# Optimization experiments

Measured on AMD Instinct MI355X. Metric: run time of the kernel, lower is better.

## Reference

```python
import jax, jax.numpy as jnp
import numpy as np

N = 100000  # nodes
E = 500000  # directed edges (before self-loops)

def _glorot(key, fi, fo):
    s = np.sqrt(6.0 / (fi + fo)).astype(np.float32)
    return jax.random.uniform(key, (fi, fo), jnp.float32, -s, s)

def setup_inputs() -> dict:
    key = jax.random.key(0)
    ks = jax.random.split(key, 6)
    x = jax.random.normal(ks[0], (N, 128), jnp.float32)
    edge_index = jax.random.randint(ks[1], (2, E), 0, N, dtype=jnp.int64)
    return {
        "x": x,
        "edge_index": edge_index,
        "W1": _glorot(ks[2], 128, 512), "b1": jnp.zeros((512,), jnp.float32),
        "W2": _glorot(ks[3], 512, 768), "b2": jnp.zeros((768,), jnp.float32),
        "W3": _glorot(ks[4], 768, 512), "b3": jnp.zeros((512,), jnp.float32),
        "W4": _glorot(ks[5], 512, 128), "b4": jnp.zeros((128,), jnp.float32),
    }

def reference(x, edge_index, W1, b1, W2, b2, W3, b3, W4, b4):
    # PyG GCNConv: add self-loops, deg from dst index, sym-normalized scatter-add.
    loops = jnp.arange(N, dtype=edge_index.dtype)
    src = jnp.concatenate([edge_index[0], loops])  # [E+N]
    dst = jnp.concatenate([edge_index[1], loops])  # [E+N]
    deg = jax.ops.segment_sum(jnp.ones_like(dst, jnp.float32), dst, num_segments=N)
    dinv = jax.lax.rsqrt(deg)  # deg >= 1 thanks to self-loops
    norm = (dinv[src] * dinv[dst])[:, None]  # [E+N, 1]

    def gcn_conv(h, W, b):
        hw = h @ W                                  # [N, Fout] dense linear
        msg = norm * hw[src]                        # [E+N, Fout] gather + scale
        return jax.ops.segment_sum(msg, dst, num_segments=N) + b

    h = jax.nn.gelu(gcn_conv(x, W1, b1), approximate=False)
    h = jax.nn.gelu(gcn_conv(h, W2, b2), approximate=False)
    h = jax.nn.gelu(gcn_conv(h, W3, b3), approximate=False)
    return gcn_conv(h, W4, b4)
```

## Files before the change

### kernel.cpp

```cpp
#include <hip/hip_runtime.h>

typedef short bf16x8 __attribute__((ext_vector_type(8)));
typedef float f32x4 __attribute__((ext_vector_type(4)));

__device__ __forceinline__ float b2f(unsigned short u) {
  union { unsigned int i; float f; } x; x.i = ((unsigned int)u) << 16; return x.f;
}
__device__ __forceinline__ unsigned short f2b(float f) {
  union { float f; unsigned int u; } x; x.f = f;
  unsigned int r = (x.u + 0x7FFFu + ((x.u >> 16) & 1u)) >> 16;
  return (unsigned short)r;
}
__device__ __forceinline__ float gelu_f(float v) {
  return 0.5f * v * (1.0f + erff(v * 0.70710678118654752440f));
}


__global__ void count_kernel(const int* __restrict__ ei, int E, int* __restrict__ cnt) {
  int e = blockIdx.x * 256 + threadIdx.x;
  if (e < E) atomicAdd(&cnt[ei[E + e]], 1);
}

__global__ void dinv_kernel(const int* __restrict__ cnt, float* __restrict__ dinv, int Nn) {
  int n = blockIdx.x * 256 + threadIdx.x;
  if (n < Nn) dinv[n] = rsqrtf((float)cnt[n] + 1.0f);
}


__global__ __launch_bounds__(256) void scanA_kernel(const int* __restrict__ cnt,
                                                    int* __restrict__ bsum, int Nn) {
  __shared__ int red[256];
  const int t = threadIdx.x;
  const int base = blockIdx.x * 512 + t * 2;
  int a = (base < Nn) ? cnt[base] : 0;
  int b = (base + 1 < Nn) ? cnt[base + 1] : 0;
  red[t] = a + b;
  __syncthreads();
  for (int d = 128; d > 0; d >>= 1) {
    if (t < d) red[t] += red[t + d];
    __syncthreads();
  }
  if (t == 0) bsum[blockIdx.x] = red[0];
}

__global__ __launch_bounds__(256) void scanB_kernel(const int* __restrict__ bsum,
                                                    int* __restrict__ boff,
                                                    int* __restrict__ rowstart,
                                                    int NBLK, int Nn) {
  __shared__ int sh[256];
  const int t = threadIdx.x;
  sh[t] = (t < NBLK) ? bsum[t] : 0;
  __syncthreads();
  for (int d = 1; d < 256; d <<= 1) {
    int x = sh[t];
    int add = (t >= d) ? sh[t - d] : 0;
    __syncthreads();
    sh[t] = x + add;
    __syncthreads();
  }
  if (t < NBLK) boff[t] = (t == 0) ? 0 : sh[t - 1];
  if (t == NBLK - 1) rowstart[Nn] = sh[t];
}

__global__ __launch_bounds__(256) void scanC_kernel(const int* __restrict__ cnt,
                                                    const int* __restrict__ boff,
                                                    int* __restrict__ rowstart,
                                                    int* __restrict__ cursor, int Nn) {
  __shared__ int sh[256];
  const int t = threadIdx.x;
  const int base = blockIdx.x * 512 + t * 2;
  int a = (base < Nn) ? cnt[base] : 0;
  int b = (base + 1 < Nn) ? cnt[base + 1] : 0;
  sh[t] = a + b;
  __syncthreads();
  for (int d = 1; d < 256; d <<= 1) {
    int x = sh[t];
    int add = (t >= d) ? sh[t - d] : 0;
    __syncthreads();
    sh[t] = x + add;
    __syncthreads();
  }
  const int off = boff[blockIdx.x] + ((t == 0) ? 0 : sh[t - 1]);
  if (base < Nn) { rowstart[base] = off; cursor[base] = off; }
  if (base + 1 < Nn) { rowstart[base + 1] = off + a; cursor[base + 1] = off + a; }
}

__global__ void fill_kernel(const int* __restrict__ ei, int E, const float* __restrict__ dinv,
                            int* __restrict__ cursor, int* __restrict__ ssrc,
                            float* __restrict__ snorm) {
  int e = blockIdx.x * 256 + threadIdx.x;
  if (e < E) {
    int s = ei[e], d = ei[E + e];
    int pos = atomicAdd(&cursor[d], 1);
    ssrc[pos] = s;
    snorm[pos] = dinv[s] * dinv[d];
  }
}

__global__ void wtrans_kernel(const float* __restrict__ W, unsigned short* __restrict__ WT,
                              int K, int N) {
  int i = blockIdx.x * 256 + threadIdx.x;
  if (i < K * N) {
    int n = i / K, k = i - n * K;
    WT[i] = f2b(W[k * N + n]);
  }
}


template <int F, bool INF32, bool OUTF32, bool HASBIAS, bool DOGELU>
__global__ __launch_bounds__(256) void agg_kernel(
    const int* __restrict__ rowstart, const int* __restrict__ ssrc,
    const float* __restrict__ snorm, const float* __restrict__ dinv,
    const void* __restrict__ inv, const float* __restrict__ bias,
    void* __restrict__ outv, int Nn) {
  constexpr int V = F / 64;
  const int lane = threadIdx.x & 63;
  const int node = blockIdx.x * 4 + (threadIdx.x >> 6);
  if (node >= Nn) return;
  const int base = lane * V;
  float acc[V];
  {
    float w = dinv[node]; w = w * w;
    if constexpr (INF32) {
      const float* in = (const float*)inv + (size_t)node * F + base;
      if constexpr (V == 2) {
        float2 v = *(const float2*)in; acc[0] = w * v.x; acc[1] = w * v.y;
      } else {
        float4 v0 = *(const float4*)in; float4 v1 = *(const float4*)(in + 4);
        acc[0] = w * v0.x; acc[1] = w * v0.y; acc[2] = w * v0.z; acc[3] = w * v0.w;
        acc[4] = w * v1.x; acc[5] = w * v1.y; acc[6] = w * v1.z; acc[7] = w * v1.w;
      }
    } else {
      const unsigned short* in = (const unsigned short*)inv + (size_t)node * F + base;
      if constexpr (V == 2) {
        unsigned int v = *(const unsigned int*)in;
        acc[0] = w * b2f(v & 0xffffu); acc[1] = w * b2f(v >> 16);
      } else {
        bf16x8 v = *(const bf16x8*)in;
#pragma unroll
        for (int i = 0; i < 8; ++i) acc[i] = w * b2f((unsigned short)v[i]);
      }
    }
  }
  const int e0 = rowstart[node], e1 = rowstart[node + 1];
  for (int e = e0; e < e1; ++e) {
    const int s = ssrc[e];
    const float w = snorm[e];
    if constexpr (INF32) {
      const float* in = (const float*)inv + (size_t)s * F + base;
      if constexpr (V == 2) {
        float2 v = *(const float2*)in; acc[0] += w * v.x; acc[1] += w * v.y;
      } else {
        float4 v0 = *(const float4*)in; float4 v1 = *(const float4*)(in + 4);
        acc[0] += w * v0.x; acc[1] += w * v0.y; acc[2] += w * v0.z; acc[3] += w * v0.w;
        acc[4] += w * v1.x; acc[5] += w * v1.y; acc[6] += w * v1.z; acc[7] += w * v1.w;
      }
    } else {
      const unsigned short* in = (const unsigned short*)inv + (size_t)s * F + base;
      if constexpr (V == 2) {
        unsigned int v = *(const unsigned int*)in;
        acc[0] += w * b2f(v & 0xffffu); acc[1] += w * b2f(v >> 16);
      } else {
        bf16x8 v = *(const bf16x8*)in;
#pragma unroll
        for (int i = 0; i < 8; ++i) acc[i] += w * b2f((unsigned short)v[i]);
      }
    }
  }
  if constexpr (HASBIAS) {
#pragma unroll
    for (int i = 0; i < V; ++i) acc[i] += bias[base + i];
  }
  if constexpr (DOGELU) {
#pragma unroll
    for (int i = 0; i < V; ++i) acc[i] = gelu_f(acc[i]);
  }
  if constexpr (OUTF32) {
    float* out = (float*)outv + (size_t)node * F + base;
#pragma unroll
    for (int i = 0; i < V; ++i) out[i] = acc[i];
  } else {
    unsigned short* out = (unsigned short*)outv + (size_t)node * F + base;
    if constexpr (V == 2) {
      unsigned int pack = (unsigned int)f2b(acc[0]) | ((unsigned int)f2b(acc[1]) << 16);
      *(unsigned int*)out = pack;
    } else {
      bf16x8 o;
#pragma unroll
      for (int i = 0; i < 8; ++i) o[i] = (short)f2b(acc[i]);
      *(bf16x8*)out = o;
    }
  }
}


template <bool HASBIAS, bool DOGELU>
__global__ __launch_bounds__(512, 2) void gemm256(
    const unsigned short* __restrict__ A, const unsigned short* __restrict__ BT,
    const float* __restrict__ bias, unsigned short* __restrict__ C,
    int N, int K, int NT) {
  __shared__ alignas(16) unsigned short smem[65536];
  unsigned short* As = smem;
  unsigned short* Bs = smem + 32768;
  const int tid = threadIdx.x;
  const int lane = tid & 63;
  const int wid = tid >> 6;
  const int wr = wid >> 2;
  const int wc = wid & 3;
  const int rr = lane & 15, rg = lane >> 4;

  const int G = gridDim.x;
  const int q = G >> 3, r = G & 7;
  const int xcd = blockIdx.x & 7, ii = blockIdx.x >> 3;
  const int w = (xcd < r ? xcd * (q + 1) : r * (q + 1) + (xcd - r) * q) + ii;
  const int bx = w / NT;
  const int by = w - bx * NT;
  const size_t brow = (size_t)bx * 256;
  const size_t bcol = (size_t)by * 256;

  const int nt = K >> 6;

  auto stage = [&](int t) {
    const int kb = t << 6;
    const int buf = t & 1;
#pragma unroll
    for (int j = 0; j < 4; ++j) {
      const int s = tid + 512 * j;
      const int row = s >> 3;
      const int lslot = (s & 7) ^ (row & 7);
      const unsigned short* gA = A + (brow + row) * K + kb + lslot * 8;
      __builtin_amdgcn_global_load_lds((const __attribute__((address_space(1))) void*)gA,
          (__attribute__((address_space(3))) void*)(&As[buf * 16384 + s * 8]), 16, 0, 0);
      const unsigned short* gB = BT + (bcol + row) * K + kb + lslot * 8;
      __builtin_amdgcn_global_load_lds((const __attribute__((address_space(1))) void*)gB,
          (__attribute__((address_space(3))) void*)(&Bs[buf * 16384 + s * 8]), 16, 0, 0);
    }
  };

  f32x4 acc[8][4] = {};
  stage(0);
  __syncthreads();
  for (int t = 0; t < nt; ++t) {
    if (t + 1 < nt) stage(t + 1);
    const int buf = t & 1;
    bf16x8 bq[2][4];
#pragma unroll
    for (int kk = 0; kk < 2; ++kk)
#pragma unroll
      for (int nb = 0; nb < 4; ++nb) {
        const int R = wc * 64 + nb * 16 + rr;
        const int ps = (kk * 4 + rg) ^ (R & 7);
        bq[kk][nb] = *(const bf16x8*)(&Bs[buf * 16384 + R * 64 + ps * 8]);
      }
#pragma unroll
    for (int mb = 0; mb < 8; ++mb) {
      const int R = wr * 128 + mb * 16 + rr;
      const int ps0 = rg ^ (R & 7);
      const int ps1 = (4 + rg) ^ (R & 7);
      bf16x8 a0 = *(const bf16x8*)(&As[buf * 16384 + R * 64 + ps0 * 8]);
      bf16x8 a1 = *(const bf16x8*)(&As[buf * 16384 + R * 64 + ps1 * 8]);
#pragma unroll
      for (int nb = 0; nb < 4; ++nb)
        acc[mb][nb] = __builtin_amdgcn_mfma_f32_16x16x32_bf16(a0, bq[0][nb], acc[mb][nb], 0, 0, 0);
#pragma unroll
      for (int nb = 0; nb < 4; ++nb)
        acc[mb][nb] = __builtin_amdgcn_mfma_f32_16x16x32_bf16(a1, bq[1][nb], acc[mb][nb], 0, 0, 0);
    }
    __syncthreads();
  }

  char* Cl = (char*)smem;
#pragma unroll
  for (int mb = 0; mb < 8; ++mb) {
    const int rowl0 = wr * 128 + mb * 16 + rg * 4;
#pragma unroll
    for (int nb = 0; nb < 4; ++nb) {
      const int coll = wc * 64 + nb * 16 + rr;
      float bv = 0.0f;
      if constexpr (HASBIAS) bv = bias[bcol + coll];
#pragma unroll
      for (int r2 = 0; r2 < 4; ++r2) {
        float v = acc[mb][nb][r2] + bv;
        if constexpr (DOGELU) v = gelu_f(v);
        const int rowl = rowl0 + r2;
        *(unsigned short*)(Cl + rowl * 512 + ((coll * 2) ^ ((rowl & 7) << 4))) = f2b(v);
      }
    }
  }
  __syncthreads();
#pragma unroll
  for (int pass = 0; pass < 2; ++pass) {
    const int rowl = pass * 128 + (tid >> 2);
    const int u = tid & 3;
    const size_t gbase = (brow + rowl) * (size_t)N + bcol;
#pragma unroll
    for (int c = 0; c < 8; ++c) {
      uint4 v = *(const uint4*)(Cl + rowl * 512 + ((c * 64 + u * 16) ^ ((rowl & 7) << 4)));
      *(uint4*)(&C[gbase + c * 32 + u * 8]) = v;
    }
  }
}


template <bool HASBIAS, bool DOGELU>
__global__ __launch_bounds__(256) void gemm_bt(
    const unsigned short* __restrict__ A, const unsigned short* __restrict__ BT,
    const float* __restrict__ bias, unsigned short* __restrict__ C,
    int N, int K, int NT) {
  __shared__ alignas(16) unsigned short Asl[128 * 32];
  __shared__ alignas(16) unsigned short Bsl[128 * 32];
  const int tid = threadIdx.x;
  const int lane = tid & 63;
  const int wid = tid >> 6;

  const int G = gridDim.x;
  const int q = G >> 3, r = G & 7;
  const int xcd = blockIdx.x & 7, ii = blockIdx.x >> 3;
  const int w = (xcd < r ? xcd * (q + 1) : r * (q + 1) + (xcd - r) * q) + ii;
  const int bx = w / NT;
  const int by = w - bx * NT;

  const size_t brow = (size_t)bx * 128;
  const size_t bcol = (size_t)by * 128;
  const int wr = (wid >> 1) * 64;
  const int wc = (wid & 1) * 64;
  const int rr = lane & 15, rg = lane >> 4;
  f32x4 acc[4][4] = {};
  const int KT = K >> 5;
  for (int kt = 0; kt < KT; ++kt) {
    const int kb = kt << 5;
#pragma unroll
    for (int rsub = 0; rsub < 2; ++rsub) {
      const int c = tid + rsub * 256;
      const int arow = c >> 2;
      const int jlog = (c & 3) ^ ((arow >> 1) & 3);
      const unsigned short* gA = A + (brow + arow) * K + kb + jlog * 8;
      __builtin_amdgcn_global_load_lds((const __attribute__((address_space(1))) void*)gA,
                                       (__attribute__((address_space(3))) void*)(&Asl[c * 8]),
                                       16, 0, 0);
      const unsigned short* gB = BT + (bcol + arow) * K + kb + jlog * 8;
      __builtin_amdgcn_global_load_lds((const __attribute__((address_space(1))) void*)gB,
                                       (__attribute__((address_space(3))) void*)(&Bsl[c * 8]),
                                       16, 0, 0);
    }
    __syncthreads();
    bf16x8 af[4], bfr[4];
#pragma unroll
    for (int m = 0; m < 4; ++m) {
      const int R = wr + m * 16 + rr;
      af[m] = *(const bf16x8*)(&Asl[R * 32 + ((rg ^ ((R >> 1) & 3)) * 8)]);
    }
#pragma unroll
    for (int n = 0; n < 4; ++n) {
      const int R = wc + n * 16 + rr;
      bfr[n] = *(const bf16x8*)(&Bsl[R * 32 + ((rg ^ ((R >> 1) & 3)) * 8)]);
    }
#pragma unroll
    for (int m = 0; m < 4; ++m)
#pragma unroll
      for (int n = 0; n < 4; ++n)
        acc[m][n] = __builtin_amdgcn_mfma_f32_16x16x32_bf16(af[m], bfr[n], acc[m][n], 0, 0, 0);
    __syncthreads();
  }
#pragma unroll
  for (int m = 0; m < 4; ++m) {
    size_t row0 = brow + wr + m * 16 + rg * 4;
#pragma unroll
    for (int n = 0; n < 4; ++n) {
      size_t col = bcol + wc + n * 16 + rr;
      float bv = 0.0f;
      if constexpr (HASBIAS) bv = bias[col];
#pragma unroll
      for (int r2 = 0; r2 < 4; ++r2) {
        float v = acc[m][n][r2] + bv;
        if constexpr (DOGELU) v = gelu_f(v);
        C[(row0 + r2) * N + col] = f2b(v);
      }
    }
  }
}


extern "C" void kernel_launch(void* const* d_in, const int* in_sizes, int n_in,
                              void* d_out, int out_size, void* d_ws, size_t ws_size,
                              hipStream_t stream) {
  const float* x = (const float*)d_in[0];
  const int* ei = (const int*)d_in[1];
  const float* W1 = (const float*)d_in[2]; const float* b1 = (const float*)d_in[3];
  const float* W2 = (const float*)d_in[4]; const float* b2 = (const float*)d_in[5];
  const float* W3 = (const float*)d_in[6]; const float* b3 = (const float*)d_in[7];
  const float* W4 = (const float*)d_in[8]; const float* b4 = (const float*)d_in[9];

  const int Nn = in_sizes[0] / 128;
  const int E = in_sizes[1] / 2;
  const int Mpad = (Nn + 255) & ~255;

  char* p = (char*)d_ws;
  auto alloc = [&](size_t bytes) {
    char* r = p;
    p += (bytes + 255) & ~(size_t)255;
    return r;
  };
  float* dinv = (float*)alloc((size_t)Nn * 4);
  int* cnt = (int*)alloc((size_t)Nn * 4);
  int* rowstart = (int*)alloc((size_t)(Nn + 1) * 4);
  int* cursor = (int*)alloc((size_t)Nn * 4);
  int* ssrc = (int*)alloc((size_t)E * 4);
  float* snorm = (float*)alloc((size_t)E * 4);
  int* bsum = (int*)alloc((size_t)256 * 4);
  int* boff = (int*)alloc((size_t)256 * 4);
  unsigned short* WT1 = (unsigned short*)alloc((size_t)512 * 128 * 2);
  unsigned short* WT2 = (unsigned short*)alloc((size_t)768 * 512 * 2);
  unsigned short* WT3 = (unsigned short*)alloc((size_t)512 * 768 * 2);
  unsigned short* WT4 = (unsigned short*)alloc((size_t)128 * 512 * 2);
  unsigned short* bufA = (unsigned short*)alloc((size_t)Mpad * 512 * 2);
  unsigned short* bufB = (unsigned short*)alloc((size_t)Mpad * 768 * 2);

  const int EB = (E + 255) / 256;
  const int NB = (Nn + 255) / 256;
  const int AGGB = (Nn + 3) / 4;
  const int MT128 = Mpad / 128;
  const int MT256 = Mpad / 256;
  const int NSCAN = (Nn + 511) / 512;

  hipMemsetAsync(cnt, 0, (size_t)Nn * 4, stream);
  count_kernel<<<EB, 256, 0, stream>>>(ei, E, cnt);
  dinv_kernel<<<NB, 256, 0, stream>>>(cnt, dinv, Nn);
  scanA_kernel<<<NSCAN, 256, 0, stream>>>(cnt, bsum, Nn);
  scanB_kernel<<<1, 256, 0, stream>>>(bsum, boff, rowstart, NSCAN, Nn);
  scanC_kernel<<<NSCAN, 256, 0, stream>>>(cnt, boff, rowstart, cursor, Nn);
  fill_kernel<<<EB, 256, 0, stream>>>(ei, E, dinv, cursor, ssrc, snorm);
  wtrans_kernel<<<(128 * 512 + 255) / 256, 256, 0, stream>>>(W1, WT1, 128, 512);
  wtrans_kernel<<<(512 * 768 + 255) / 256, 256, 0, stream>>>(W2, WT2, 512, 768);
  wtrans_kernel<<<(768 * 512 + 255) / 256, 256, 0, stream>>>(W3, WT3, 768, 512);
  wtrans_kernel<<<(512 * 128 + 255) / 256, 256, 0, stream>>>(W4, WT4, 512, 128);

  agg_kernel<128, true, false, false, false><<<AGGB, 256, 0, stream>>>(
      rowstart, ssrc, snorm, dinv, x, nullptr, bufA, Nn);
  gemm256<true, true><<<MT256 * 2, 512, 0, stream>>>(bufA, WT1, b1, bufB, 512, 128, 2);

  agg_kernel<512, false, false, false, false><<<AGGB, 256, 0, stream>>>(
      rowstart, ssrc, snorm, dinv, bufB, nullptr, bufA, Nn);
  gemm256<true, true><<<MT256 * 3, 512, 0, stream>>>(bufA, WT2, b2, bufB, 768, 512, 3);

  gemm256<false, false><<<MT256 * 2, 512, 0, stream>>>(bufB, WT3, nullptr, bufA, 512, 768, 2);
  agg_kernel<512, false, false, true, true><<<AGGB, 256, 0, stream>>>(
      rowstart, ssrc, snorm, dinv, bufA, b3, bufB, Nn);

  gemm_bt<false, false><<<MT128 * 1, 256, 0, stream>>>(bufB, WT4, nullptr, bufA, 128, 512, 1);
  agg_kernel<128, false, true, true, false><<<AGGB, 256, 0, stream>>>(
      rowstart, ssrc, snorm, dinv, bufA, b4, d_out, Nn);
}
```

Measured before the change: 781.9 us.

## Restructure gemm256 main loop into fine-grained phased pipeline with explicit waitcnts

The 256x256 GEMM main loop is rewritten as eight phases per 128-wide K step. Each phase loads a quarter-size A or B half-tile into LDS while the MFMAs for the previous sub-tile run, using explicit vmcnt waits, raw s_barrier and s_setprio instead of one full-tile prefetch followed by __syncthreads. The LDS layout changes to 32-wide K halves with a new XOR swizzle, and launch bounds drop to one block per CU to free registers. The goal is to hide global-to-LDS latency and barrier stalls behind MFMA work. The hand-counted waitcnt scheme assumes K is a multiple of 128 and the exact number of loads in flight, so it is fragile.

```diff
diff --git a/kernel.cpp b/kernel.cpp
--- a/kernel.cpp
+++ b/kernel.cpp
@@ -194,14 +194,16 @@
 }
 
 
+#define GLOAD16(gp, lp)                                                              \
+  __builtin_amdgcn_global_load_lds((const __attribute__((address_space(1))) void*)(gp), \
+                                   (__attribute__((address_space(3))) void*)(lp), 16, 0, 0)
+
 template <bool HASBIAS, bool DOGELU>
-__global__ __launch_bounds__(512, 2) void gemm256(
+__global__ __launch_bounds__(512, 1) void gemm256(
     const unsigned short* __restrict__ A, const unsigned short* __restrict__ BT,
     const float* __restrict__ bias, unsigned short* __restrict__ C,
     int N, int K, int NT) {
   __shared__ alignas(16) unsigned short smem[65536];
-  unsigned short* As = smem;
-  unsigned short* Bs = smem + 32768;
   const int tid = threadIdx.x;
   const int lane = tid & 63;
   const int wid = tid >> 6;
@@ -218,56 +220,94 @@
   const size_t brow = (size_t)bx * 256;
   const size_t bcol = (size_t)by * 256;
 
-  const int nt = K >> 6;
-
-  auto stage = [&](int t) {
-    const int kb = t << 6;
-    const int buf = t & 1;
-#pragma unroll
-    for (int j = 0; j < 4; ++j) {
+  const int ntiles = K >> 6;
+  const int NIT = K >> 7;
+
+  auto stageA = [&](int tl, int h) {
+    if (tl >= ntiles) return;
+    const int kb = (tl << 6) + (h << 5);
+    unsigned short* dst = smem + ((tl & 1) * 2 + h) * 8192;
+#pragma unroll
+    for (int j = 0; j < 2; ++j) {
       const int s = tid + 512 * j;
-      const int row = s >> 3;
-      const int lslot = (s & 7) ^ (row & 7);
-      const unsigned short* gA = A + (brow + row) * K + kb + lslot * 8;
-      __builtin_amdgcn_global_load_lds((const __attribute__((address_space(1))) void*)gA,
-          (__attribute__((address_space(3))) void*)(&As[buf * 16384 + s * 8]), 16, 0, 0);
-      const unsigned short* gB = BT + (bcol + row) * K + kb + lslot * 8;
-      __builtin_amdgcn_global_load_lds((const __attribute__((address_space(1))) void*)gB,
-          (__attribute__((address_space(3))) void*)(&Bs[buf * 16384 + s * 8]), 16, 0, 0);
+      const int row = s >> 2;
+      const int kof = (((s & 3) ^ ((row >> 1) & 3)) << 3);
+      GLOAD16(A + (brow + row) * K + kb + kof, dst + s * 8);
     }
   };
+  auto stageB = [&](int tl, int h) {
+    if (tl >= ntiles) return;
+    const int kb = (tl << 6) + (h << 5);
+    unsigned short* dst = smem + 32768 + ((tl & 1) * 2 + h) * 8192;
+#pragma unroll
+    for (int j = 0; j < 2; ++j) {
+      const int s = tid + 512 * j;
+      const int row = s >> 2;
+      const int kof = (((s & 3) ^ ((row >> 1) & 3)) << 3);
+      GLOAD16(BT + (bcol + row) * K + kb + kof, dst + s * 8);
+    }
+  };
 
   f32x4 acc[8][4] = {};
-  stage(0);
-  __syncthreads();
-  for (int t = 0; t < nt; ++t) {
-    if (t + 1 < nt) stage(t + 1);
-    const int buf = t & 1;
-    bf16x8 bq[2][4];
-#pragma unroll
-    for (int kk = 0; kk < 2; ++kk)
-#pragma unroll
-      for (int nb = 0; nb < 4; ++nb) {
-        const int R = wc * 64 + nb * 16 + rr;
-        const int ps = (kk * 4 + rg) ^ (R & 7);
-        bq[kk][nb] = *(const bf16x8*)(&Bs[buf * 16384 + R * 64 + ps * 8]);
-      }
-#pragma unroll
-    for (int mb = 0; mb < 8; ++mb) {
-      const int R = wr * 128 + mb * 16 + rr;
-      const int ps0 = rg ^ (R & 7);
-      const int ps1 = (4 + rg) ^ (R & 7);
-      bf16x8 a0 = *(const bf16x8*)(&As[buf * 16384 + R * 64 + ps0 * 8]);
-      bf16x8 a1 = *(const bf16x8*)(&As[buf * 16384 + R * 64 + ps1 * 8]);
-#pragma unroll
-      for (int nb = 0; nb < 4; ++nb)
-        acc[mb][nb] = __builtin_amdgcn_mfma_f32_16x16x32_bf16(a0, bq[0][nb], acc[mb][nb], 0, 0, 0);
-#pragma unroll
-      for (int nb = 0; nb < 4; ++nb)
-        acc[mb][nb] = __builtin_amdgcn_mfma_f32_16x16x32_bf16(a1, bq[1][nb], acc[mb][nb], 0, 0, 0);
-    }
-    __syncthreads();
-  }
+  bf16x8 bq[4];
+
+#define PHASE(d, h, mb0, RB, STAGE_STMT)                                               \
+  do {                                                                                 \
+    const unsigned short* Ab = smem + ((d) * 2 + (h)) * 8192;                          \
+    const unsigned short* Bb = smem + 32768 + ((d) * 2 + (h)) * 8192;                  \
+    bf16x8 av[4];                                                                      \
+    if (RB) {                                                                          \
+      _Pragma("unroll") for (int nb = 0; nb < 4; ++nb) {                               \
+        const int Cc = wc * 64 + nb * 16 + rr;                                         \
+        bq[nb] = *(const bf16x8*)(Bb + Cc * 32 + ((rg ^ ((Cc >> 1) & 3)) << 3));       \
+      }                                                                                \
+    }                                                                                  \
+    _Pragma("unroll") for (int i2 = 0; i2 < 4; ++i2) {                                 \
+      const int R = wr * 128 + ((mb0) + i2) * 16 + rr;                                 \
+      av[i2] = *(const bf16x8*)(Ab + R * 32 + ((rg ^ ((R >> 1) & 3)) << 3));           \
+    }                                                                                  \
+    STAGE_STMT;                                                                        \
+    __builtin_amdgcn_s_barrier();                                                      \
+    asm volatile("s_waitcnt lgkmcnt(0)" ::: "memory");                                 \
+    __builtin_amdgcn_s_setprio(1);                                                     \
+    _Pragma("unroll") for (int i2 = 0; i2 < 4; ++i2)                                   \
+        _Pragma("unroll") for (int nb = 0; nb < 4; ++nb)                               \
+            acc[(mb0) + i2][nb] = __builtin_amdgcn_mfma_f32_16x16x32_bf16(             \
+                av[i2], bq[nb], acc[(mb0) + i2][nb], 0, 0, 0);                         \
+    __builtin_amdgcn_s_setprio(0);                                                     \
+  } while (0)
+
+  stageA(0, 0); stageB(0, 0); stageA(0, 1); stageB(0, 1); stageA(1, 0); stageB(1, 0);
+  asm volatile("s_waitcnt vmcnt(8)" ::: "memory");
+  __builtin_amdgcn_s_barrier();
+
+  for (int I = 0; I < NIT; ++I) {
+    const int t = I * 2;
+    const bool last = (I == NIT - 1);
+    PHASE(0, 0, 0, true, stageA(t + 1, 1));
+    __builtin_amdgcn_s_barrier();
+    PHASE(0, 0, 4, false, stageB(t + 1, 1));
+    asm volatile("s_waitcnt vmcnt(6)" ::: "memory");
+    __builtin_amdgcn_s_barrier();
+    PHASE(0, 1, 0, true, stageA(t + 2, 0));
+    __builtin_amdgcn_s_barrier();
+    PHASE(0, 1, 4, false, stageB(t + 2, 0));
+    if (last) asm volatile("s_waitcnt vmcnt(2)" ::: "memory");
+    else      asm volatile("s_waitcnt vmcnt(6)" ::: "memory");
+    __builtin_amdgcn_s_barrier();
+    PHASE(1, 0, 0, true, stageA(t + 2, 1));
+    __builtin_amdgcn_s_barrier();
+    PHASE(1, 0, 4, false, stageB(t + 2, 1));
+    if (last) asm volatile("s_waitcnt vmcnt(0)" ::: "memory");
+    else      asm volatile("s_waitcnt vmcnt(6)" ::: "memory");
+    __builtin_amdgcn_s_barrier();
+    PHASE(1, 1, 0, true, stageA(t + 3, 0));
+    __builtin_amdgcn_s_barrier();
+    PHASE(1, 1, 4, false, stageB(t + 3, 0));
+    if (!last) asm volatile("s_waitcnt vmcnt(6)" ::: "memory");
+    __builtin_amdgcn_s_barrier();
+  }
+#undef PHASE
 
   char* Cl = (char*)smem;
 #pragma unroll
@@ -335,13 +375,9 @@
       const int arow = c >> 2;
       const int jlog = (c & 3) ^ ((arow >> 1) & 3);
       const unsigned short* gA = A + (brow + arow) * K + kb + jlog * 8;
-      __builtin_amdgcn_global_load_lds((const __attribute__((address_space(1))) void*)gA,
-                                       (__attribute__((address_space(3))) void*)(&Asl[c * 8]),
-                                       16, 0, 0);
+      GLOAD16(gA, &Asl[c * 8]);
       const unsigned short* gB = BT + (bcol + arow) * K + kb + jlog * 8;
-      __builtin_amdgcn_global_load_lds((const __attribute__((address_space(1))) void*)gB,
-                                       (__attribute__((address_space(3))) void*)(&Bsl[c * 8]),
-                                       16, 0, 0);
+      GLOAD16(gB, &Bsl[c * 8]);
     }
     __syncthreads();
     bf16x8 af[4], bfr[4];
```

New measurement: 784.0 us. No clear change (+0.3%).

## Split 512-wide aggregation across two waves per node, unroll gathers, cast x to bf16

Applied to the files above, without the earlier changes.

The 512-feature aggregation kernels now assign two wavefronts to each destination node. Each wave handles alternating edges with two gathers in flight, and the partial sums are combined through shared memory. The 128-feature aggregation unrolls its edge loop by four so that more independent row loads are outstanding. A new cast kernel converts x to bf16 so the first aggregation gathers half the bytes, at the cost of an extra pass over x and bf16 rounding of the input features.

```diff
diff --git a/kernel.cpp b/kernel.cpp
--- a/kernel.cpp
+++ b/kernel.cpp
@@ -24,6 +24,19 @@
 __global__ void dinv_kernel(const int* __restrict__ cnt, float* __restrict__ dinv, int Nn) {
   int n = blockIdx.x * 256 + threadIdx.x;
   if (n < Nn) dinv[n] = rsqrtf((float)cnt[n] + 1.0f);
+}
+
+__global__ void xcast_kernel(const float* __restrict__ x, unsigned short* __restrict__ xb,
+                             int total8) {
+  int i = blockIdx.x * 256 + threadIdx.x;
+  if (i < total8) {
+    float4 a = *(const float4*)(x + (size_t)i * 8);
+    float4 b = *(const float4*)(x + (size_t)i * 8 + 4);
+    bf16x8 o;
+    o[0] = (short)f2b(a.x); o[1] = (short)f2b(a.y); o[2] = (short)f2b(a.z); o[3] = (short)f2b(a.w);
+    o[4] = (short)f2b(b.x); o[5] = (short)f2b(b.y); o[6] = (short)f2b(b.z); o[7] = (short)f2b(b.w);
+    *(bf16x8*)(xb + (size_t)i * 8) = o;
+  }
 }
 
 
@@ -107,66 +120,116 @@
 }
 
 
-template <int F, bool INF32, bool OUTF32, bool HASBIAS, bool DOGELU>
+template <int F, bool INF32>
+__device__ __forceinline__ void rowload(const void* inv, int row, int base, float* r) {
+  constexpr int V = F / 64;
+  if constexpr (INF32) {
+    const float* in = (const float*)inv + (size_t)row * F + base;
+    if constexpr (V == 2) {
+      float2 v = *(const float2*)in; r[0] = v.x; r[1] = v.y;
+    } else {
+      float4 v0 = *(const float4*)in; float4 v1 = *(const float4*)(in + 4);
+      r[0] = v0.x; r[1] = v0.y; r[2] = v0.z; r[3] = v0.w;
+      r[4] = v1.x; r[5] = v1.y; r[6] = v1.z; r[7] = v1.w;
+    }
+  } else {
+    const unsigned short* in = (const unsigned short*)inv + (size_t)row * F + base;
+    if constexpr (V == 2) {
+      unsigned int v = *(const unsigned int*)in;
+      r[0] = b2f(v & 0xffffu); r[1] = b2f(v >> 16);
+    } else {
+      bf16x8 v = *(const bf16x8*)in;
+#pragma unroll
+      for (int i = 0; i < 8; ++i) r[i] = b2f((unsigned short)v[i]);
+    }
+  }
+}
+
+template <int F, int WPN, bool INF32, bool OUTF32, bool HASBIAS, bool DOGELU>
 __global__ __launch_bounds__(256) void agg_kernel(
     const int* __restrict__ rowstart, const int* __restrict__ ssrc,
     const float* __restrict__ snorm, const float* __restrict__ dinv,
     const void* __restrict__ inv, const float* __restrict__ bias,
     void* __restrict__ outv, int Nn) {
   constexpr int V = F / 64;
+  constexpr int NPB = 4 / WPN;
   const int lane = threadIdx.x & 63;
-  const int node = blockIdx.x * 4 + (threadIdx.x >> 6);
-  if (node >= Nn) return;
+  const int wid = threadIdx.x >> 6;
+  const int nslot = wid / WPN;
+  const int sub = wid % WPN;
+  const int node = blockIdx.x * NPB + nslot;
+  constexpr int CMBSZ = (WPN > 1) ? (NPB * F) : 1;
+  __shared__ float cmb[CMBSZ];
+
   const int base = lane * V;
   float acc[V];
-  {
-    float w = dinv[node]; w = w * w;
-    if constexpr (INF32) {
-      const float* in = (const float*)inv + (size_t)node * F + base;
-      if constexpr (V == 2) {
-        float2 v = *(const float2*)in; acc[0] = w * v.x; acc[1] = w * v.y;
-      } else {
-        float4 v0 = *(const float4*)in; float4 v1 = *(const float4*)(in + 4);
-        acc[0] = w * v0.x; acc[1] = w * v0.y; acc[2] = w * v0.z; acc[3] = w * v0.w;
-        acc[4] = w * v1.x; acc[5] = w * v1.y; acc[6] = w * v1.z; acc[7] = w * v1.w;
+#pragma unroll
+  for (int i = 0; i < V; ++i) acc[i] = 0.0f;
+
+  if (node < Nn) {
+    if (sub == 0) {
+      float w = dinv[node]; w = w * w;
+      float rv[V];
+      rowload<F, INF32>(inv, node, base, rv);
+#pragma unroll
+      for (int i = 0; i < V; ++i) acc[i] = w * rv[i];
+    }
+    const int e0 = rowstart[node], e1 = rowstart[node + 1];
+    int e = e0 + sub;
+    if constexpr (WPN == 1) {
+      for (; e + 4 <= e1; e += 4) {
+        int si[4]; float wi[4];
+#pragma unroll
+        for (int u = 0; u < 4; ++u) { si[u] = ssrc[e + u]; wi[u] = snorm[e + u]; }
+        float rv[4][V];
+#pragma unroll
+        for (int u = 0; u < 4; ++u) rowload<F, INF32>(inv, si[u], base, rv[u]);
+#pragma unroll
+        for (int u = 0; u < 4; ++u)
+#pragma unroll
+          for (int i = 0; i < V; ++i) acc[i] += wi[u] * rv[u][i];
+      }
+      for (; e < e1; ++e) {
+        const int s = ssrc[e];
+        const float w = snorm[e];
+        float rv[V];
+        rowload<F, INF32>(inv, s, base, rv);
+#pragma unroll
+        for (int i = 0; i < V; ++i) acc[i] += w * rv[i];
       }
     } else {
-      const unsigned short* in = (const unsigned short*)inv + (size_t)node * F + base;
-      if constexpr (V == 2) {
-        unsigned int v = *(const unsigned int*)in;
-        acc[0] = w * b2f(v & 0xffffu); acc[1] = w * b2f(v >> 16);
-      } else {
-        bf16x8 v = *(const bf16x8*)in;
-#pragma unroll
-        for (int i = 0; i < 8; ++i) acc[i] = w * b2f((unsigned short)v[i]);
-      }
-    }
-  }
-  const int e0 = rowstart[node], e1 = rowstart[node + 1];
-  for (int e = e0; e < e1; ++e) {
-    const int s = ssrc[e];
-    const float w = snorm[e];
-    if constexpr (INF32) {
-      const float* in = (const float*)inv + (size_t)s * F + base;
-      if constexpr (V == 2) {
-        float2 v = *(const float2*)in; acc[0] += w * v.x; acc[1] += w * v.y;
-      } else {
-        float4 v0 = *(const float4*)in; float4 v1 = *(const float4*)(in + 4);
-        acc[0] += w * v0.x; acc[1] += w * v0.y; acc[2] += w * v0.z; acc[3] += w * v0.w;
-        acc[4] += w * v1.x; acc[5] += w * v1.y; acc[6] += w * v1.z; acc[7] += w * v1.w;
-      }
-    } else {
-      const unsigned short* in = (const unsigned short*)inv + (size_t)s * F + base;
-      if constexpr (V == 2) {
-        unsigned int v = *(const unsigned int*)in;
-        acc[0] += w * b2f(v & 0xffffu); acc[1] += w * b2f(v >> 16);
-      } else {
-        bf16x8 v = *(const bf16x8*)in;
-#pragma unroll
-        for (int i = 0; i < 8; ++i) acc[i] += w * b2f((unsigned short)v[i]);
-      }
-    }
-  }
+      for (; e + WPN < e1; e += 2 * WPN) {
+        int s0 = ssrc[e], s1 = ssrc[e + WPN];
+        float w0 = snorm[e], w1 = snorm[e + WPN];
+        float r0[V], r1[V];
+        rowload<F, INF32>(inv, s0, base, r0);
+        rowload<F, INF32>(inv, s1, base, r1);
+#pragma unroll
+        for (int i = 0; i < V; ++i) acc[i] += w0 * r0[i] + w1 * r1[i];
+      }
+      if (e < e1) {
+        const int s = ssrc[e];
+        const float w = snorm[e];
+        float rv[V];
+        rowload<F, INF32>(inv, s, base, rv);
+#pragma unroll
+        for (int i = 0; i < V; ++i) acc[i] += w * rv[i];
+      }
+    }
+  }
+
+  if constexpr (WPN > 1) {
+    if (sub == 1) {
+#pragma unroll
+      for (int i = 0; i < V; ++i) cmb[nslot * F + base + i] = acc[i];
+    }
+    __syncthreads();
+    if (sub != 0) return;
+#pragma unroll
+    for (int i = 0; i < V; ++i) acc[i] += cmb[nslot * F + base + i];
+  }
+  if (node >= Nn || sub != 0) return;
+
   if constexpr (HASBIAS) {
 #pragma unroll
     for (int i = 0; i < V; ++i) acc[i] += bias[base + i];
@@ -193,6 +256,10 @@
   }
 }
 
+
+#define GLOAD16(gp, lp)                                                              \
+  __builtin_amdgcn_global_load_lds((const __attribute__((address_space(1))) void*)(gp), \
+                                   (__attribute__((address_space(3))) void*)(lp), 16, 0, 0)
 
 template <bool HASBIAS, bool DOGELU>
 __global__ __launch_bounds__(512, 2) void gemm256(
@@ -228,12 +295,8 @@
       const int s = tid + 512 * j;
       const int row = s >> 3;
       const int lslot = (s & 7) ^ (row & 7);
-      const unsigned short* gA = A + (brow + row) * K + kb + lslot * 8;
-      __builtin_amdgcn_global_load_lds((const __attribute__((address_space(1))) void*)gA,
-          (__attribute__((address_space(3))) void*)(&As[buf * 16384 + s * 8]), 16, 0, 0);
-      const unsigned short* gB = BT + (bcol + row) * K + kb + lslot * 8;
-      __builtin_amdgcn_global_load_lds((const __attribute__((address_space(1))) void*)gB,
-          (__attribute__((address_space(3))) void*)(&Bs[buf * 16384 + s * 8]), 16, 0, 0);
+      GLOAD16(A + (brow + row) * K + kb + lslot * 8, &As[buf * 16384 + s * 8]);
+      GLOAD16(BT + (bcol + row) * K + kb + lslot * 8, &Bs[buf * 16384 + s * 8]);
     }
   };
 
@@ -334,14 +397,8 @@
       const int c = tid + rsub * 256;
       const int arow = c >> 2;
       const int jlog = (c & 3) ^ ((arow >> 1) & 3);
-      const unsigned short* gA = A + (brow + arow) * K + kb + jlog * 8;
-      __builtin_amdgcn_global_load_lds((const __attribute__((address_space(1))) void*)gA,
-                                       (__attribute__((address_space(3))) void*)(&Asl[c * 8]),
-                                       16, 0, 0);
-      const unsigned short* gB = BT + (bcol + arow) * K + kb + jlog * 8;
-      __builtin_amdgcn_global_load_lds((const __attribute__((address_space(1))) void*)gB,
-                                       (__attribute__((address_space(3))) void*)(&Bsl[c * 8]),
-                                       16, 0, 0);
+      GLOAD16(A + (brow + arow) * K + kb + jlog * 8, &Asl[c * 8]);
+      GLOAD16(BT + (bcol + arow) * K + kb + jlog * 8, &Bsl[c * 8]);
     }
     __syncthreads();
     bf16x8 af[4], bfr[4];
@@ -415,12 +472,12 @@
   unsigned short* WT4 = (unsigned short*)alloc((size_t)128 * 512 * 2);
   unsigned short* bufA = (unsigned short*)alloc((size_t)Mpad * 512 * 2);
   unsigned short* bufB = (unsigned short*)alloc((size_t)Mpad * 768 * 2);
+  unsigned short* xb = bufB;
 
   const int EB = (E + 255) / 256;
   const int NB = (Nn + 255) / 256;
-  const int AGGB = (Nn + 3) / 4;
+  const int MT256 = Mpad / 256;
   const int MT128 = Mpad / 128;
-  const int MT256 = Mpad / 256;
   const int NSCAN = (Nn + 511) / 512;
 
   hipMemsetAsync(cnt, 0, (size_t)Nn * 4, stream);
@@ -434,20 +491,21 @@
   wtrans_kernel<<<(512 * 768 + 255) / 256, 256, 0, stream>>>(W2, WT2, 512, 768);
   wtrans_kernel<<<(768 * 512 + 255) / 256, 256, 0, stream>>>(W3, WT3, 768, 512);
   wtrans_kernel<<<(512 * 128 + 255) / 256, 256, 0, stream>>>(W4, WT4, 512, 128);
-
-  agg_kernel<128, true, false, false, false><<<AGGB, 256, 0, stream>>>(
-      rowstart, ssrc, snorm, dinv, x, nullptr, bufA, Nn);
+  xcast_kernel<<<(Nn * 16 + 255) / 256, 256, 0, stream>>>(x, xb, Nn * 16);
+
+  agg_kernel<128, 1, false, false, false, false><<<(Nn + 3) / 4, 256, 0, stream>>>(
+      rowstart, ssrc, snorm, dinv, xb, nullptr, bufA, Nn);
   gemm256<true, true><<<MT256 * 2, 512, 0, stream>>>(bufA, WT1, b1, bufB, 512, 128, 2);
 
-  agg_kernel<512, false, false, false, false><<<AGGB, 256, 0, stream>>>(
+  agg_kernel<512, 2, false, false, false, false><<<(Nn + 1) / 2, 256, 0, stream>>>(
       rowstart, ssrc, snorm, dinv, bufB, nullptr, bufA, Nn);
   gemm256<true, true><<<MT256 * 3, 512, 0, stream>>>(bufA, WT2, b2, bufB, 768, 512, 3);
 
   gemm256<false, false><<<MT256 * 2, 512, 0, stream>>>(bufB, WT3, nullptr, bufA, 512, 768, 2);
-  agg_kernel<512, false, false, true, true><<<AGGB, 256, 0, stream>>>(
+  agg_kernel<512, 2, false, false, true, true><<<(Nn + 1) / 2, 256, 0, stream>>>(
       rowstart, ssrc, snorm, dinv, bufA, b3, bufB, Nn);
 
   gemm_bt<false, false><<<MT128 * 1, 256, 0, stream>>>(bufB, WT4, nullptr, bufA, 128, 512, 1);
-  agg_kernel<128, false, true, true, false><<<AGGB, 256, 0, stream>>>(
+  agg_kernel<128, 1, false, true, true, false><<<(Nn + 3) / 4, 256, 0, stream>>>(
       rowstart, ssrc, snorm, dinv, bufA, b4, d_out, Nn);
 }
```

Measured after the change: 739.9 us. 1.06x faster.
